# Kernel optimization log

Measured on AMD Instinct MI355X. Metric: run time of the kernel, lower is better.

## Reference

```python
import jax, jax.numpy as jnp
import numpy as np

N_EMBD = 768
N_HEAD = 12

def setup_inputs() -> dict:
    key = jax.random.key(0)
    ks = jax.random.split(key, 10)
    B, T, C = 2, 2048, N_EMBD
    s = 1.0 / np.sqrt(C)
    x = jax.random.normal(ks[0], (B, T, C), dtype=jnp.float32)
    attn_mask = jnp.ones((B, 1, T, T), dtype=jnp.float32)
    Wq = jax.random.normal(ks[1], (C, C), dtype=jnp.float32) * s
    bq = jax.random.normal(ks[2], (C,), dtype=jnp.float32) * 0.01
    Wk = jax.random.normal(ks[3], (C, C), dtype=jnp.float32) * s
    bk = jax.random.normal(ks[4], (C,), dtype=jnp.float32) * 0.01
    Wv = jax.random.normal(ks[5], (C, C), dtype=jnp.float32) * s
    bv = jax.random.normal(ks[6], (C,), dtype=jnp.float32) * 0.01
    Wp = jax.random.normal(ks[7], (C, C), dtype=jnp.float32) * s
    bp = jax.random.normal(ks[8], (C,), dtype=jnp.float32) * 0.01
    return {"x": x, "attn_mask": attn_mask, "Wq": Wq, "bq": bq, "Wk": Wk, "bk": bk,
            "Wv": Wv, "bv": bv, "Wp": Wp, "bp": bp}

def reference(x, attn_mask, Wq, bq, Wk, bk, Wv, bv, Wp, bp):
    B, T, C = x.shape
    H = N_HEAD
    hd = C // H
    # Linear layers (torch nn.Linear: y = x @ W.T + b)
    q = (x @ Wq.T + bq).reshape(B, T, H, hd).transpose(0, 2, 1, 3)  # [B,H,T,hd]
    k = (x @ Wk.T + bk).reshape(B, T, H, hd).transpose(0, 2, 1, 3)
    v = (x @ Wv.T + bv).reshape(B, T, H, hd).transpose(0, 2, 1, 3)
    att = jnp.einsum('bhqd,bhkd->bhqk', q, k) / jnp.sqrt(jnp.float32(hd))  # [B,H,T,T]
    causal = jnp.tril(jnp.ones((T, T), dtype=jnp.bool_))[None, None]       # [1,1,T,T]
    combined = causal & (attn_mask > 0)                                    # broadcast to [B,H,T,T]
    att = jnp.where(combined, att, -jnp.inf)
    att = jax.nn.softmax(att, axis=-1)
    y = jnp.einsum('bhqk,bhkd->bhqd', att, v)                              # [B,H,T,hd]
    y = y.transpose(0, 2, 1, 3).reshape(B, T, C)
    return y @ Wp.T + bp
```

## Files before the change

kernel.cpp:

```cpp
#include <hip/hip_runtime.h>
#include <hip/hip_bf16.h>
#include <cstdint>
#include <cstddef>

#define B_   2
#define H_   12
#define T_   2048
#define C_   768
#define HD_  64
#define M_   4096
#define NW_  (T_/64)

typedef __attribute__((ext_vector_type(8))) short bf16x8;
typedef __attribute__((ext_vector_type(4))) float fx4;
typedef __attribute__((ext_vector_type(16))) float f32x16;
typedef unsigned short u16;
typedef unsigned int   u32;
typedef unsigned long long u64;

static __device__ __forceinline__ u16 f2bf(float f){
    union { float f; unsigned int i; } c; c.f = f;
    unsigned int x = c.i;
    return (u16)((x + 0x7fffu + ((x >> 16) & 1u)) >> 16);
}

static __device__ __forceinline__ u32 pack_bf2(float a, float b){
    union { __hip_bfloat162 h; u32 u; } cv;
    cv.h = __float22bfloat162_rn(make_float2(a, b));
    return cv.u;
}

__global__ void cvt_f32_bf16(const float* __restrict__ src, u16* __restrict__ dst, int n4){
    int i = blockIdx.x * blockDim.x + threadIdx.x;
    if (i < n4){
        float4 v = ((const float4*)src)[i];
        ushort4 o;
        o.x = f2bf(v.x); o.y = f2bf(v.y); o.z = f2bf(v.z); o.w = f2bf(v.w);
        ((ushort4*)dst)[i] = o;
    }
}

__global__ void cvt_w4(const float* __restrict__ wq, const float* __restrict__ wk,
                       const float* __restrict__ wv, const float* __restrict__ wp,
                       u16* __restrict__ dst){
    const float* src = (blockIdx.y == 0) ? wq : (blockIdx.y == 1) ? wk
                     : (blockIdx.y == 2) ? wv : wp;
    int i = blockIdx.x * blockDim.x + threadIdx.x;
    float4 v = ((const float4*)src)[i];
    ushort4 o;
    o.x = f2bf(v.x); o.y = f2bf(v.y); o.z = f2bf(v.z); o.w = f2bf(v.w);
    ((ushort4*)(dst + (size_t)blockIdx.y * C_ * C_))[i] = o;
}

__global__ void mask_bits_kernel(const float* __restrict__ mask, u64* __restrict__ bits){
    int wid  = blockIdx.x * (blockDim.x >> 6) + (threadIdx.x >> 6);
    int lane = threadIdx.x & 63;
    float v = mask[(size_t)wid * 64 + lane];
    u64 m = __ballot(v > 0.0f);
    if (lane == 0) bits[wid] = m;
}

__launch_bounds__(256, 2)
__global__ void gemm_qkv(const u16* __restrict__ xb, const u16* __restrict__ wqkv,
                         const float* __restrict__ bq, const float* __restrict__ bk,
                         const float* __restrict__ bv,
                         u16* __restrict__ qo, u16* __restrict__ ko, u16* __restrict__ vto)
{
    const int tid  = threadIdx.x;
    const int lane = tid & 63, wave = tid >> 6;
    const int l15 = lane & 15, lg = lane >> 4;
    int flat = blockIdx.x + 6 * (blockIdx.y + 32 * blockIdx.z);
    int swz  = (flat & 7) * 72 + (flat >> 3);
    const int n0 = (swz % 6) * 128;
    const int m0 = ((swz / 6) % 32) * 128;
    const int z  = swz / 192;
    const u16* wb     = wqkv + (size_t)z * C_ * C_;
    const float* bias = (z == 0) ? bq : (z == 1 ? bk : bv);
    const float oscl  = (z == 0) ? 0.1803368801111601f : 1.0f;

    __shared__ __align__(16) u16 lds_a[128 * 64];
    __shared__ __align__(16) u16 lds_b[128 * 64];

    fx4 acc[4][4];
    #pragma unroll
    for (int i = 0; i < 4; i++)
        #pragma unroll
        for (int j = 0; j < 4; j++) acc[i][j] = (fx4)0.0f;

    const int wm = (wave >> 1) * 64, wn = (wave & 1) * 64;
    const int sx = l15 & 7;

    for (int kt = 0; kt < C_ / 64; ++kt){
        const int k0 = kt * 64;
        #pragma unroll
        for (int c = 0; c < 4; ++c){
            int unit = c * 256 + tid;
            int row = unit >> 3, col = unit & 7;
            int gcol = (col ^ (row & 7)) * 8;
            const u16* ga = xb + (size_t)(m0 + row) * C_ + k0 + gcol;
            __builtin_amdgcn_global_load_lds((const __attribute__((address_space(1))) void*)ga,
                (__attribute__((address_space(3))) void*)(lds_a + (c * 256 + wave * 64) * 8), 16, 0, 0);
            const u16* gb = wb + (size_t)(n0 + row) * C_ + k0 + gcol;
            __builtin_amdgcn_global_load_lds((const __attribute__((address_space(1))) void*)gb,
                (__attribute__((address_space(3))) void*)(lds_b + (c * 256 + wave * 64) * 8), 16, 0, 0);
        }
        __syncthreads();
        #pragma unroll
        for (int ks = 0; ks < 2; ++ks){
            bf16x8 af[4], bfr[4];
            #pragma unroll
            for (int i = 0; i < 4; i++){
                af[i]  = *(const bf16x8*)&lds_a[(wm + i * 16 + l15) * 64 + (((4 * ks + lg) ^ sx) * 8)];
                bfr[i] = *(const bf16x8*)&lds_b[(wn + i * 16 + l15) * 64 + (((4 * ks + lg) ^ sx) * 8)];
            }
            #pragma unroll
            for (int i = 0; i < 4; i++)
                #pragma unroll
                for (int j = 0; j < 4; j++)
                    acc[i][j] = __builtin_amdgcn_mfma_f32_16x16x32_bf16(af[i], bfr[j], acc[i][j], 0, 0, 0);
        }
        __syncthreads();
    }

    #pragma unroll
    for (int i = 0; i < 4; i++){
        #pragma unroll
        for (int j = 0; j < 4; j++){
            #pragma unroll
            for (int r = 0; r < 4; r++){
                int m = m0 + wm + i * 16 + lg * 4 + r;
                int n = n0 + wn + j * 16 + l15;
                float v = (acc[i][j][r] + bias[n]) * oscl;
                u16 o = f2bf(v);
                int b = m >> 11, t = m & (T_ - 1);
                int h = n >> 6, d = n & 63;
                if (z == 2){
                    vto[(size_t)((b * H_ + h) * HD_ + d) * T_ + t] = o;
                } else {
                    u16* dst = (z == 0) ? qo : ko;
                    dst[(size_t)((b * H_ + h) * T_ + t) * HD_ + d] = o;
                }
            }
        }
    }
}

__launch_bounds__(256, 2)
__global__ void gemm_proj(const u16* __restrict__ yb, const u16* __restrict__ wp,
                          const float* __restrict__ bp, float* __restrict__ out)
{
    const int tid  = threadIdx.x;
    const int lane = tid & 63, wave = tid >> 6;
    const int l15 = lane & 15, lg = lane >> 4;
    int flat = blockIdx.x + 6 * blockIdx.y;
    int swz  = (flat & 7) * 24 + (flat >> 3);
    const int n0 = (swz % 6) * 128;
    const int m0 = (swz / 6) * 128;

    __shared__ __align__(16) u16 lds_a[128 * 64];
    __shared__ __align__(16) u16 lds_b[128 * 64];

    fx4 acc[4][4];
    #pragma unroll
    for (int i = 0; i < 4; i++)
        #pragma unroll
        for (int j = 0; j < 4; j++) acc[i][j] = (fx4)0.0f;

    const int wm = (wave >> 1) * 64, wn = (wave & 1) * 64;
    const int sx = l15 & 7;

    for (int kt = 0; kt < C_ / 64; ++kt){
        const int k0 = kt * 64;
        #pragma unroll
        for (int c = 0; c < 4; ++c){
            int unit = c * 256 + tid;
            int row = unit >> 3, col = unit & 7;
            int gcol = (col ^ (row & 7)) * 8;
            const u16* ga = yb + (size_t)(m0 + row) * C_ + k0 + gcol;
            __builtin_amdgcn_global_load_lds((const __attribute__((address_space(1))) void*)ga,
                (__attribute__((address_space(3))) void*)(lds_a + (c * 256 + wave * 64) * 8), 16, 0, 0);
            const u16* gb = wp + (size_t)(n0 + row) * C_ + k0 + gcol;
            __builtin_amdgcn_global_load_lds((const __attribute__((address_space(1))) void*)gb,
                (__attribute__((address_space(3))) void*)(lds_b + (c * 256 + wave * 64) * 8), 16, 0, 0);
        }
        __syncthreads();
        #pragma unroll
        for (int ks = 0; ks < 2; ++ks){
            bf16x8 af[4], bfr[4];
            #pragma unroll
            for (int i = 0; i < 4; i++){
                af[i]  = *(const bf16x8*)&lds_a[(wm + i * 16 + l15) * 64 + (((4 * ks + lg) ^ sx) * 8)];
                bfr[i] = *(const bf16x8*)&lds_b[(wn + i * 16 + l15) * 64 + (((4 * ks + lg) ^ sx) * 8)];
            }
            #pragma unroll
            for (int i = 0; i < 4; i++)
                #pragma unroll
                for (int j = 0; j < 4; j++)
                    acc[i][j] = __builtin_amdgcn_mfma_f32_16x16x32_bf16(af[i], bfr[j], acc[i][j], 0, 0, 0);
        }
        __syncthreads();
    }

    #pragma unroll
    for (int i = 0; i < 4; i++)
        #pragma unroll
        for (int j = 0; j < 4; j++)
            #pragma unroll
            for (int r = 0; r < 4; r++){
                int m = m0 + wm + i * 16 + lg * 4 + r;
                int n = n0 + wn + j * 16 + l15;
                out[(size_t)m * C_ + n] = acc[i][j][r] + bp[n];
            }
}

__launch_bounds__(128, 2)
__global__ void attn(const u16* __restrict__ q, const u16* __restrict__ kmat,
                     const u16* __restrict__ vt, const u64* __restrict__ bits,
                     u16* __restrict__ y)
{
    const int tid = threadIdx.x, lane = tid & 63, w = tid >> 6;
    const int l31 = lane & 31, hi = lane >> 5;
    int flat = blockIdx.x;
    const int bh = (flat & 7) * 3 + ((flat >> 3) % 3);
    const int qt = 31 - (flat >> 3) / 3;
    const int b = bh / H_, h = bh % H_;
    const int q0 = qt * 64;
    const int qw0 = q0 + 32 * w;

    __shared__ __align__(16) u16 lds_k[64 * 64];
    __shared__ __align__(16) u16 lds_v[64 * 64];

    const size_t bhoff = (size_t)bh * T_ * HD_;

    bf16x8 qf[4];
    {
        const u16* qrow = q + bhoff + (size_t)(qw0 + l31) * HD_ + hi * 8;
        #pragma unroll
        for (int dc = 0; dc < 4; dc++)
            qf[dc] = *(const bf16x8*)(qrow + dc * 16);
    }

    f32x16 o0 = (f32x16)0.0f, o1 = (f32x16)0.0f;
    float m_l = -1e30f, l_l = 0.0f;

    const int nkt = qt + 1;
    const int qg  = qw0 + l31;
    const u64* brow = bits + (size_t)(b * T_ + qg) * NW_;

    const int sr = tid >> 3;
    const int sc = tid & 7;

    bf16x8 kreg[4], vreg[4];
    {
        #pragma unroll
        for (int i = 0; i < 4; i++){
            int row = sr + 16 * i;
            kreg[i] = *(const bf16x8*)(kmat + bhoff + (size_t)row * HD_ + sc * 8);
            vreg[i] = *(const bf16x8*)(vt   + bhoff + (size_t)row * T_  + sc * 8);
        }
        #pragma unroll
        for (int i = 0; i < 4; i++){
            int row = sr + 16 * i;
            *(bf16x8*)&lds_k[row * 64 + ((sc ^ (row & 7)) * 8)] = kreg[i];
            *(bf16x8*)&lds_v[row * 64 + ((sc ^ (row & 7)) * 8)] = vreg[i];
        }
    }
    __syncthreads();

    for (int kt = 0; kt < nkt; ++kt){
        const int kbase = kt * 64;
        const bool pf = (kt + 1 < nkt);
        if (pf){
            const int kb2 = kbase + 64;
            #pragma unroll
            for (int i = 0; i < 4; i++){
                int row = sr + 16 * i;
                kreg[i] = *(const bf16x8*)(kmat + bhoff + (size_t)(kb2 + row) * HD_ + sc * 8);
                vreg[i] = *(const bf16x8*)(vt   + bhoff + (size_t)row * T_ + kb2 + sc * 8);
            }
        }

        f32x16 s0 = (f32x16)0.0f, s1 = (f32x16)0.0f;
        #pragma unroll
        for (int dc = 0; dc < 4; dc++){
            bf16x8 kf0 = *(const bf16x8*)&lds_k[(l31     ) * 64 + (((2 * dc + hi) ^ (l31 & 7)) * 8)];
            bf16x8 kf1 = *(const bf16x8*)&lds_k[(l31 + 32) * 64 + (((2 * dc + hi) ^ (l31 & 7)) * 8)];
            s0 = __builtin_amdgcn_mfma_f32_32x32x16_bf16(kf0, qf[dc], s0, 0, 0, 0);
            s1 = __builtin_amdgcn_mfma_f32_32x32x16_bf16(kf1, qf[dc], s1, 0, 0, 0);
        }

        u64 raw = brow[kt];
        int sh = qg - kbase;
        u64 vis = sh < 0 ? 0ull : (sh >= 63 ? ~0ull : ((2ull << sh) - 1ull));
        u64 masked = raw & vis;
        if (!__all(masked == ~0ull)){
            u32 mk0 = (u32)(masked >> (4 * hi));
            u32 mk1 = (u32)(masked >> (32 + 4 * hi));
            #pragma unroll
            for (int r = 0; r < 16; r++){
                int bpos = (r & 3) + 8 * (r >> 2);
                s0[r] = ((mk0 >> bpos) & 1u) ? s0[r] : -1e30f;
                s1[r] = ((mk1 >> bpos) & 1u) ? s1[r] : -1e30f;
            }
        }

        float mx = -1e30f;
        #pragma unroll
        for (int r = 0; r < 16; r++){ mx = fmaxf(mx, s0[r]); mx = fmaxf(mx, s1[r]); }
        mx = fmaxf(mx, __shfl_xor(mx, 32, 64));

        if (!__all(mx <= m_l + 10.0f)){
            float mnew = fmaxf(m_l, mx);
            float al = __builtin_amdgcn_exp2f(m_l - mnew);
            m_l = mnew;
            l_l *= al;
            #pragma unroll
            for (int r = 0; r < 16; r++){
                int ql = (r & 3) + 8 * (r >> 2) + 4 * hi;
                float a_r = __shfl(al, ql, 64);
                o0[r] *= a_r; o1[r] *= a_r;
            }
        }

        float rs = 0.0f;
        bf16x8 pa[2][2];
        #pragma unroll
        for (int kb = 0; kb < 2; kb++){
            u32 P[8];
            #pragma unroll
            for (int g = 0; g < 8; g++){
                float pe0 = __builtin_amdgcn_exp2f((kb ? s1[2*g]   : s0[2*g])   - m_l);
                float pe1 = __builtin_amdgcn_exp2f((kb ? s1[2*g+1] : s0[2*g+1]) - m_l);
                rs += pe0 + pe1;
                P[g] = pack_bf2(pe0, pe1);
            }
            asm volatile("v_permlane32_swap_b32 %0, %1" : "+v"(P[0]), "+v"(P[2]));
            asm volatile("v_permlane32_swap_b32 %0, %1" : "+v"(P[1]), "+v"(P[3]));
            asm volatile("v_permlane32_swap_b32 %0, %1" : "+v"(P[4]), "+v"(P[6]));
            asm volatile("v_permlane32_swap_b32 %0, %1" : "+v"(P[5]), "+v"(P[7]));
            union { u32 uw[4]; bf16x8 v; } u0, u1;
            u0.uw[0]=P[0]; u0.uw[1]=P[1]; u0.uw[2]=P[2]; u0.uw[3]=P[3];
            u1.uw[0]=P[4]; u1.uw[1]=P[5]; u1.uw[2]=P[6]; u1.uw[3]=P[7];
            pa[kb][0] = u0.v; pa[kb][1] = u1.v;
        }
        rs += __shfl_xor(rs, 32, 64);
        l_l += rs;

        #pragma unroll
        for (int kb = 0; kb < 2; kb++)
            #pragma unroll
            for (int ks = 0; ks < 2; ks++){
                int gidx = 4 * kb + 2 * ks + hi;
                bf16x8 vf0 = *(const bf16x8*)&lds_v[(l31     ) * 64 + ((gidx ^ (l31 & 7)) * 8)];
                bf16x8 vf1 = *(const bf16x8*)&lds_v[(l31 + 32) * 64 + ((gidx ^ (l31 & 7)) * 8)];
                o0 = __builtin_amdgcn_mfma_f32_32x32x16_bf16(pa[kb][ks], vf0, o0, 0, 0, 0);
                o1 = __builtin_amdgcn_mfma_f32_32x32x16_bf16(pa[kb][ks], vf1, o1, 0, 0, 0);
            }

        if (pf){
            __syncthreads();
            #pragma unroll
            for (int i = 0; i < 4; i++){
                int row = sr + 16 * i;
                *(bf16x8*)&lds_k[row * 64 + ((sc ^ (row & 7)) * 8)] = kreg[i];
                *(bf16x8*)&lds_v[row * 64 + ((sc ^ (row & 7)) * 8)] = vreg[i];
            }
            __syncthreads();
        }
    }

    float inv = 1.0f / l_l;
    #pragma unroll
    for (int r = 0; r < 16; r++){
        int ql = (r & 3) + 8 * (r >> 2) + 4 * hi;
        float iv = __shfl(inv, ql, 64);
        int trow = qw0 + ql;
        u16* yr = y + (size_t)(b * T_ + trow) * C_ + h * HD_;
        yr[l31]      = f2bf(o0[r] * iv);
        yr[32 + l31] = f2bf(o1[r] * iv);
    }
}

extern "C" void kernel_launch(void* const* d_in, const int* in_sizes, int n_in,
                              void* d_out, int out_size, void* d_ws, size_t ws_size,
                              hipStream_t stream)
{
    const float* x    = (const float*)d_in[0];
    const float* mask = (const float*)d_in[1];
    const float* Wq   = (const float*)d_in[2];
    const float* bq   = (const float*)d_in[3];
    const float* Wk   = (const float*)d_in[4];
    const float* bk   = (const float*)d_in[5];
    const float* Wv   = (const float*)d_in[6];
    const float* bv   = (const float*)d_in[7];
    const float* Wp   = (const float*)d_in[8];
    const float* bp   = (const float*)d_in[9];
    float* out = (float*)d_out;

    char* p = (char*)d_ws;
    u16* xb   = (u16*)p; p += (size_t)M_ * C_ * 2;
    u16* wqkv = (u16*)p; p += (size_t)4 * C_ * C_ * 2;
    u16* qo   = (u16*)p; p += (size_t)M_ * C_ * 2;
    u16* ko   = (u16*)p; p += (size_t)M_ * C_ * 2;
    u16* vto  = (u16*)p; p += (size_t)M_ * C_ * 2;
    u16* yb   = (u16*)p; p += (size_t)M_ * C_ * 2;
    u64* bits = (u64*)p; p += (size_t)B_ * T_ * NW_ * 8;

    const int NX4 = M_ * C_ / 4;
    const int NW4 = C_ * C_ / 4;
    cvt_f32_bf16<<<dim3((NX4 + 255) / 256), 256, 0, stream>>>(x, xb, NX4);
    cvt_w4<<<dim3(NW4 / 256, 4), 256, 0, stream>>>(Wq, Wk, Wv, Wp, wqkv);
    mask_bits_kernel<<<dim3(B_ * T_ * NW_ / 4), 256, 0, stream>>>(mask, bits);

    gemm_qkv<<<dim3(C_ / 128, M_ / 128, 3), 256, 0, stream>>>(
        xb, wqkv, bq, bk, bv, qo, ko, vto);

    attn<<<dim3((T_ / 64) * B_ * H_), 128, 0, stream>>>(qo, ko, vto, bits, yb);

    gemm_proj<<<dim3(C_ / 128, M_ / 128), 256, 0, stream>>>(yb, wqkv + (size_t)3 * C_ * C_, bp, out);
}
```

Baseline: 130.0 us.

## Split attention KV loop across four wave-pairs per block with LDS merge

Each attention block now runs four independent wave-pairs (512 threads). Each pair handles an interleaved subset of the causal K/V tiles with its own LDS buffers. At the end the pairs' partial outputs and max/sum statistics are merged through shared memory into one softmax-normalised result. This adds parallelism for the long causal rows and cuts the serial tile loop per wave. In exchange it adds a merge phase and more LDS, and the (512,4) launch bound may sharply restrict registers per thread and cause spills.

New measurement: 149.0 us. 14.6% more time.

```diff
diff --git a/kernel.cpp b/kernel.cpp
--- a/kernel.cpp
+++ b/kernel.cpp
@@ -10,6 +10,7 @@
 #define HD_  64
 #define M_   4096
 #define NW_  (T_/64)
+#define NPAIR 4
 
 typedef __attribute__((ext_vector_type(8))) short bf16x8;
 typedef __attribute__((ext_vector_type(4))) float fx4;
@@ -213,22 +214,28 @@
             }
 }
 
-__launch_bounds__(128, 2)
+__launch_bounds__(512, 4)
 __global__ void attn(const u16* __restrict__ q, const u16* __restrict__ kmat,
                      const u16* __restrict__ vt, const u64* __restrict__ bits,
                      u16* __restrict__ y)
 {
-    const int tid = threadIdx.x, lane = tid & 63, w = tid >> 6;
+    const int tid = threadIdx.x;
+    const int pr  = tid >> 7;
+    const int ptid = tid & 127;
+    const int w2  = ptid >> 6;
+    const int lane = tid & 63;
     const int l31 = lane & 31, hi = lane >> 5;
+
     int flat = blockIdx.x;
     const int bh = (flat & 7) * 3 + ((flat >> 3) % 3);
     const int qt = 31 - (flat >> 3) / 3;
     const int b = bh / H_, h = bh % H_;
-    const int q0 = qt * 64;
-    const int qw0 = q0 + 32 * w;
-
-    __shared__ __align__(16) u16 lds_k[64 * 64];
-    __shared__ __align__(16) u16 lds_v[64 * 64];
+    const int qw0 = qt * 64 + 32 * w2;
+
+    extern __shared__ __align__(16) u16 smem[];
+    u16* lds_k = smem + (size_t)pr * 8192;
+    u16* lds_v = smem + (size_t)pr * 8192 + 4096;
+    float* lds_ml = (float*)smem;
 
     const size_t bhoff = (size_t)bh * T_ * HD_;
 
@@ -244,19 +251,21 @@
     float m_l = -1e30f, l_l = 0.0f;
 
     const int nkt = qt + 1;
+    const int nit = (nkt + NPAIR - 1) / NPAIR;
     const int qg  = qw0 + l31;
     const u64* brow = bits + (size_t)(b * T_ + qg) * NW_;
 
-    const int sr = tid >> 3;
-    const int sc = tid & 7;
+    const int sr = ptid >> 3;
+    const int sc = ptid & 7;
 
     bf16x8 kreg[4], vreg[4];
-    {
+    if (pr < nkt){
+        const int kb0 = pr * 64;
         #pragma unroll
         for (int i = 0; i < 4; i++){
             int row = sr + 16 * i;
-            kreg[i] = *(const bf16x8*)(kmat + bhoff + (size_t)row * HD_ + sc * 8);
-            vreg[i] = *(const bf16x8*)(vt   + bhoff + (size_t)row * T_  + sc * 8);
+            kreg[i] = *(const bf16x8*)(kmat + bhoff + (size_t)(kb0 + row) * HD_ + sc * 8);
+            vreg[i] = *(const bf16x8*)(vt   + bhoff + (size_t)row * T_ + kb0 + sc * 8);
         }
         #pragma unroll
         for (int i = 0; i < 4; i++){
@@ -267,11 +276,12 @@
     }
     __syncthreads();
 
-    for (int kt = 0; kt < nkt; ++kt){
-        const int kbase = kt * 64;
-        const bool pf = (kt + 1 < nkt);
+    for (int it = 0; it < nit; ++it){
+        const int kt = it * NPAIR + pr;
+        const bool valid = kt < nkt;
+        const bool pf = kt + NPAIR < nkt;
         if (pf){
-            const int kb2 = kbase + 64;
+            const int kb2 = (kt + NPAIR) * 64;
             #pragma unroll
             for (int i = 0; i < 4; i++){
                 int row = sr + 16 * i;
@@ -280,104 +290,160 @@
             }
         }
 
-        f32x16 s0 = (f32x16)0.0f, s1 = (f32x16)0.0f;
-        #pragma unroll
-        for (int dc = 0; dc < 4; dc++){
-            bf16x8 kf0 = *(const bf16x8*)&lds_k[(l31     ) * 64 + (((2 * dc + hi) ^ (l31 & 7)) * 8)];
-            bf16x8 kf1 = *(const bf16x8*)&lds_k[(l31 + 32) * 64 + (((2 * dc + hi) ^ (l31 & 7)) * 8)];
-            s0 = __builtin_amdgcn_mfma_f32_32x32x16_bf16(kf0, qf[dc], s0, 0, 0, 0);
-            s1 = __builtin_amdgcn_mfma_f32_32x32x16_bf16(kf1, qf[dc], s1, 0, 0, 0);
-        }
-
-        u64 raw = brow[kt];
-        int sh = qg - kbase;
-        u64 vis = sh < 0 ? 0ull : (sh >= 63 ? ~0ull : ((2ull << sh) - 1ull));
-        u64 masked = raw & vis;
-        if (!__all(masked == ~0ull)){
-            u32 mk0 = (u32)(masked >> (4 * hi));
-            u32 mk1 = (u32)(masked >> (32 + 4 * hi));
-            #pragma unroll
-            for (int r = 0; r < 16; r++){
-                int bpos = (r & 3) + 8 * (r >> 2);
-                s0[r] = ((mk0 >> bpos) & 1u) ? s0[r] : -1e30f;
-                s1[r] = ((mk1 >> bpos) & 1u) ? s1[r] : -1e30f;
-            }
-        }
-
-        float mx = -1e30f;
-        #pragma unroll
-        for (int r = 0; r < 16; r++){ mx = fmaxf(mx, s0[r]); mx = fmaxf(mx, s1[r]); }
-        mx = fmaxf(mx, __shfl_xor(mx, 32, 64));
-
-        if (!__all(mx <= m_l + 10.0f)){
-            float mnew = fmaxf(m_l, mx);
-            float al = __builtin_amdgcn_exp2f(m_l - mnew);
-            m_l = mnew;
-            l_l *= al;
+        if (valid){
+            const int kbase = kt * 64;
+            f32x16 s0 = (f32x16)0.0f, s1 = (f32x16)0.0f;
+            #pragma unroll
+            for (int dc = 0; dc < 4; dc++){
+                bf16x8 kf0 = *(const bf16x8*)&lds_k[(l31     ) * 64 + (((2 * dc + hi) ^ (l31 & 7)) * 8)];
+                bf16x8 kf1 = *(const bf16x8*)&lds_k[(l31 + 32) * 64 + (((2 * dc + hi) ^ (l31 & 7)) * 8)];
+                s0 = __builtin_amdgcn_mfma_f32_32x32x16_bf16(kf0, qf[dc], s0, 0, 0, 0);
+                s1 = __builtin_amdgcn_mfma_f32_32x32x16_bf16(kf1, qf[dc], s1, 0, 0, 0);
+            }
+
+            u64 raw = brow[kt];
+            int sh = qg - kbase;
+            u64 vis = sh < 0 ? 0ull : (sh >= 63 ? ~0ull : ((2ull << sh) - 1ull));
+            u64 masked = raw & vis;
+            if (!__all(masked == ~0ull)){
+                u32 mk0 = (u32)(masked >> (4 * hi));
+                u32 mk1 = (u32)(masked >> (32 + 4 * hi));
+                #pragma unroll
+                for (int r = 0; r < 16; r++){
+                    int bpos = (r & 3) + 8 * (r >> 2);
+                    s0[r] = ((mk0 >> bpos) & 1u) ? s0[r] : -1e30f;
+                    s1[r] = ((mk1 >> bpos) & 1u) ? s1[r] : -1e30f;
+                }
+            }
+
+            float mx = -1e30f;
+            #pragma unroll
+            for (int r = 0; r < 16; r++){ mx = fmaxf(mx, s0[r]); mx = fmaxf(mx, s1[r]); }
+            mx = fmaxf(mx, __shfl_xor(mx, 32, 64));
+
+            if (!__all(mx <= m_l + 10.0f)){
+                float mnew = fmaxf(m_l, mx);
+                float al = __builtin_amdgcn_exp2f(m_l - mnew);
+                m_l = mnew;
+                l_l *= al;
+                #pragma unroll
+                for (int r = 0; r < 16; r++){
+                    int ql = (r & 3) + 8 * (r >> 2) + 4 * hi;
+                    float a_r = __shfl(al, ql, 64);
+                    o0[r] *= a_r; o1[r] *= a_r;
+                }
+            }
+
+            float rs = 0.0f;
+            bf16x8 pa[2][2];
+            #pragma unroll
+            for (int kb = 0; kb < 2; kb++){
+                u32 P[8];
+                #pragma unroll
+                for (int g = 0; g < 8; g++){
+                    float pe0 = __builtin_amdgcn_exp2f((kb ? s1[2*g]   : s0[2*g])   - m_l);
+                    float pe1 = __builtin_amdgcn_exp2f((kb ? s1[2*g+1] : s0[2*g+1]) - m_l);
+                    rs += pe0 + pe1;
+                    P[g] = pack_bf2(pe0, pe1);
+                }
+                asm volatile("v_permlane32_swap_b32 %0, %1" : "+v"(P[0]), "+v"(P[2]));
+                asm volatile("v_permlane32_swap_b32 %0, %1" : "+v"(P[1]), "+v"(P[3]));
+                asm volatile("v_permlane32_swap_b32 %0, %1" : "+v"(P[4]), "+v"(P[6]));
+                asm volatile("v_permlane32_swap_b32 %0, %1" : "+v"(P[5]), "+v"(P[7]));
+                union { u32 uw[4]; bf16x8 v; } u0, u1;
+                u0.uw[0]=P[0]; u0.uw[1]=P[1]; u0.uw[2]=P[2]; u0.uw[3]=P[3];
+                u1.uw[0]=P[4]; u1.uw[1]=P[5]; u1.uw[2]=P[6]; u1.uw[3]=P[7];
+                pa[kb][0] = u0.v; pa[kb][1] = u1.v;
+            }
+            rs += __shfl_xor(rs, 32, 64);
+            l_l += rs;
+
+            #pragma unroll
+            for (int kb = 0; kb < 2; kb++)
+                #pragma unroll
+                for (int ks = 0; ks < 2; ks++){
+                    int gidx = 4 * kb + 2 * ks + hi;
+                    bf16x8 vf0 = *(const bf16x8*)&lds_v[(l31     ) * 64 + ((gidx ^ (l31 & 7)) * 8)];
+                    bf16x8 vf1 = *(const bf16x8*)&lds_v[(l31 + 32) * 64 + ((gidx ^ (l31 & 7)) * 8)];
+                    o0 = __builtin_amdgcn_mfma_f32_32x32x16_bf16(pa[kb][ks], vf0, o0, 0, 0, 0);
+                    o1 = __builtin_amdgcn_mfma_f32_32x32x16_bf16(pa[kb][ks], vf1, o1, 0, 0, 0);
+                }
+        }
+
+        if (it + 1 < nit){
+            __syncthreads();
+            if (pf){
+                #pragma unroll
+                for (int i = 0; i < 4; i++){
+                    int row = sr + 16 * i;
+                    *(bf16x8*)&lds_k[row * 64 + ((sc ^ (row & 7)) * 8)] = kreg[i];
+                    *(bf16x8*)&lds_v[row * 64 + ((sc ^ (row & 7)) * 8)] = vreg[i];
+                }
+            }
+            __syncthreads();
+        }
+    }
+
+    __syncthreads();
+    {
+        const int qrow = w2 * 32 + l31;
+        if (hi == 0){
+            lds_ml[(pr * 2 + 0) * 64 + qrow] = m_l;
+            lds_ml[(pr * 2 + 1) * 64 + qrow] = l_l;
+        }
+        if (pr != 0){
+            float* Od = (float*)(smem + (size_t)pr * 8192);
             #pragma unroll
             for (int r = 0; r < 16; r++){
                 int ql = (r & 3) + 8 * (r >> 2) + 4 * hi;
-                float a_r = __shfl(al, ql, 64);
-                o0[r] *= a_r; o1[r] *= a_r;
-            }
-        }
-
-        float rs = 0.0f;
-        bf16x8 pa[2][2];
-        #pragma unroll
-        for (int kb = 0; kb < 2; kb++){
-            u32 P[8];
-            #pragma unroll
-            for (int g = 0; g < 8; g++){
-                float pe0 = __builtin_amdgcn_exp2f((kb ? s1[2*g]   : s0[2*g])   - m_l);
-                float pe1 = __builtin_amdgcn_exp2f((kb ? s1[2*g+1] : s0[2*g+1]) - m_l);
-                rs += pe0 + pe1;
-                P[g] = pack_bf2(pe0, pe1);
-            }
-            asm volatile("v_permlane32_swap_b32 %0, %1" : "+v"(P[0]), "+v"(P[2]));
-            asm volatile("v_permlane32_swap_b32 %0, %1" : "+v"(P[1]), "+v"(P[3]));
-            asm volatile("v_permlane32_swap_b32 %0, %1" : "+v"(P[4]), "+v"(P[6]));
-            asm volatile("v_permlane32_swap_b32 %0, %1" : "+v"(P[5]), "+v"(P[7]));
-            union { u32 uw[4]; bf16x8 v; } u0, u1;
-            u0.uw[0]=P[0]; u0.uw[1]=P[1]; u0.uw[2]=P[2]; u0.uw[3]=P[3];
-            u1.uw[0]=P[4]; u1.uw[1]=P[5]; u1.uw[2]=P[6]; u1.uw[3]=P[7];
-            pa[kb][0] = u0.v; pa[kb][1] = u1.v;
-        }
-        rs += __shfl_xor(rs, 32, 64);
-        l_l += rs;
-
-        #pragma unroll
-        for (int kb = 0; kb < 2; kb++)
-            #pragma unroll
-            for (int ks = 0; ks < 2; ks++){
-                int gidx = 4 * kb + 2 * ks + hi;
-                bf16x8 vf0 = *(const bf16x8*)&lds_v[(l31     ) * 64 + ((gidx ^ (l31 & 7)) * 8)];
-                bf16x8 vf1 = *(const bf16x8*)&lds_v[(l31 + 32) * 64 + ((gidx ^ (l31 & 7)) * 8)];
-                o0 = __builtin_amdgcn_mfma_f32_32x32x16_bf16(pa[kb][ks], vf0, o0, 0, 0, 0);
-                o1 = __builtin_amdgcn_mfma_f32_32x32x16_bf16(pa[kb][ks], vf1, o1, 0, 0, 0);
-            }
-
-        if (pf){
-            __syncthreads();
-            #pragma unroll
-            for (int i = 0; i < 4; i++){
-                int row = sr + 16 * i;
-                *(bf16x8*)&lds_k[row * 64 + ((sc ^ (row & 7)) * 8)] = kreg[i];
-                *(bf16x8*)&lds_v[row * 64 + ((sc ^ (row & 7)) * 8)] = vreg[i];
-            }
-            __syncthreads();
-        }
-    }
-
-    float inv = 1.0f / l_l;
-    #pragma unroll
-    for (int r = 0; r < 16; r++){
-        int ql = (r & 3) + 8 * (r >> 2) + 4 * hi;
-        float iv = __shfl(inv, ql, 64);
-        int trow = qw0 + ql;
-        u16* yr = y + (size_t)(b * T_ + trow) * C_ + h * HD_;
-        yr[l31]      = f2bf(o0[r] * iv);
-        yr[32 + l31] = f2bf(o1[r] * iv);
+                int row = w2 * 32 + ql;
+                Od[row * 64 + l31]      = o0[r];
+                Od[row * 64 + 32 + l31] = o1[r];
+            }
+        }
+    }
+    __syncthreads();
+
+    if (pr == 0){
+        const int qrow = w2 * 32 + l31;
+        float mvals[NPAIR], lvals[NPAIR];
+        mvals[0] = m_l; lvals[0] = l_l;
+        #pragma unroll
+        for (int p = 1; p < NPAIR; p++){
+            mvals[p] = lds_ml[(p * 2 + 0) * 64 + qrow];
+            lvals[p] = lds_ml[(p * 2 + 1) * 64 + qrow];
+        }
+        float mm = mvals[0];
+        #pragma unroll
+        for (int p = 1; p < NPAIR; p++) mm = fmaxf(mm, mvals[p]);
+        float a[NPAIR], ltot = 0.0f;
+        #pragma unroll
+        for (int p = 0; p < NPAIR; p++){
+            a[p] = __builtin_amdgcn_exp2f(mvals[p] - mm);
+            ltot += lvals[p] * a[p];
+        }
+        float inv = 1.0f / ltot;
+
+        #pragma unroll
+        for (int r = 0; r < 16; r++){
+            int ql = (r & 3) + 8 * (r >> 2) + 4 * hi;
+            int row = w2 * 32 + ql;
+            float a0r = __shfl(a[0], ql, 64);
+            float v0 = o0[r] * a0r;
+            float v1 = o1[r] * a0r;
+            #pragma unroll
+            for (int p = 1; p < NPAIR; p++){
+                float apr = __shfl(a[p], ql, 64);
+                const float* Od = (const float*)(smem + (size_t)p * 8192);
+                v0 += Od[row * 64 + l31]      * apr;
+                v1 += Od[row * 64 + 32 + l31] * apr;
+            }
+            float ivr = __shfl(inv, ql, 64);
+            int trow = qt * 64 + row;
+            u16* yr = y + (size_t)(b * T_ + trow) * C_ + h * HD_;
+            yr[l31]      = f2bf(v0 * ivr);
+            yr[32 + l31] = f2bf(v1 * ivr);
+        }
     }
 }
 
@@ -415,7 +481,8 @@
     gemm_qkv<<<dim3(C_ / 128, M_ / 128, 3), 256, 0, stream>>>(
         xb, wqkv, bq, bk, bv, qo, ko, vto);
 
-    attn<<<dim3((T_ / 64) * B_ * H_), 128, 0, stream>>>(qo, ko, vto, bits, yb);
+    attn<<<dim3((T_ / 64) * B_ * H_), 512, NPAIR * 2 * 64 * 64 * sizeof(u16), stream>>>(
+        qo, ko, vto, bits, yb);
 
     gemm_proj<<<dim3(C_ / 128, M_ / 128), 256, 0, stream>>>(yb, wqkv + (size_t)3 * C_ * C_, bp, out);
 }
```
